# Optimization experiments

Hardware: AMD Instinct MI355X
Metric: run time of the kernel (lower is better)

## Reference

```python
import jax, jax.numpy as jnp
import numpy as np

K = 11          # kernel_size
SIGMA = 1.5
CH = 3          # image channels


def _gaussian_kernel(ch):
    coords = jnp.arange(K, dtype=jnp.float32) - (K - 1) / 2
    g = jnp.exp(-coords ** 2 / (2 * SIGMA ** 2))
    g = g / g.sum()
    k2d = jnp.outer(g, g)                       # [K, K]
    return jnp.tile(k2d[None, None], (ch, 1, 1, 1))  # [C, 1, K, K] depthwise


def setup_inputs() -> dict:
    key = jax.random.key(0)
    kx, ky = jax.random.split(key)
    x = jax.random.normal(kx, (32, CH, 512, 512), dtype=jnp.float32)
    y = jax.random.normal(ky, (32, CH, 512, 512), dtype=jnp.float32)
    kernel = _gaussian_kernel(CH)
    return {"x": x, "y": y, "kernel": kernel}


def _blur(v, kernel):
    # depthwise 2D Gaussian blur, SAME padding (K odd)
    c = v.shape[1]
    pad = K // 2
    return jax.lax.conv_general_dilated(
        v, kernel, window_strides=(1, 1), padding=[(pad, pad), (pad, pad)],
        dimension_numbers=("NCHW", "OIHW", "NCHW"), feature_group_count=c)


def reference(x, y, kernel):
    C1 = 0.01 ** 2
    C2 = 0.03 ** 2
    mu_x = _blur(x, kernel)
    mu_y = _blur(y, kernel)
    sigma_x = _blur(x * x, kernel) - mu_x ** 2
    sigma_y = _blur(y * y, kernel) - mu_y ** 2
    sigma_xy = _blur(x * y, kernel) - mu_x * mu_y
    ssim_num = (2 * mu_x * mu_y + C1) * (2 * sigma_xy + C2)
    ssim_den = (mu_x ** 2 + mu_y ** 2 + C1) * (sigma_x + sigma_y + C2)
    ssim = ssim_num / (ssim_den + 1e-8)
    return ((1.0 - ssim) / 2.0).mean()
```

## Files before the change

### kernel.cpp

```cpp
#include <hip/hip_runtime.h>
#include <hip/hip_bf16.h>

#define IMG    512
#define KSZ    11
#define HALO   5
#define STRIP  64
#define PANEL  16
#define FS     20
#define CS     100
#define WRSZ   1600

typedef short bf16x8 __attribute__((ext_vector_type(8)));
typedef float f32x4  __attribute__((ext_vector_type(4)));
union S8 { bf16x8 v; ushort u16[8]; uint u32[4]; };

__device__ __forceinline__ uint cvtpk(float lo, float hi) {
    uint r;
    asm("v_cvt_pk_bf16_f32 %0, %1, %2" : "=v"(r) : "v"(lo), "v"(hi));
    return r;
}
__device__ __forceinline__ float2 pk_mul(float2 a, float2 b) {
    float2 d;
    asm("v_pk_mul_f32 %0, %1, %2" : "=v"(d) : "v"(a), "v"(b));
    return d;
}
__device__ __forceinline__ ushort f2bf(float f) {
    union { __hip_bfloat16 h; ushort u; } c;
    c.h = __float2bfloat16(f);
    return c.u;
}


__global__ __launch_bounds__(256)
void dssim_mfma_kernel(const float* __restrict__ x,
                       const float* __restrict__ y,
                       const float* __restrict__ kern,
                       float* __restrict__ out)
{
    __shared__ float  sgf[16];
    __shared__ ushort gext[64];
    __shared__ __align__(16) uint Wring[4 * WRSZ];
    __shared__ float  wsum[4];

    const int tid = threadIdx.x;
    const int l   = tid & 63;
    const int wv  = tid >> 6;
    const int q   = l >> 4;
    const int cj  = l & 15;
    const int wb  = wv * WRSZ;

    if (tid < KSZ) {
        float s = 0.f;
        #pragma unroll
        for (int j = 0; j < KSZ; ++j) s += kern[tid * KSZ + j];
        sgf[tid] = s;
    }
    for (int i = l; i < 320; i += 64) {
        const int col = i / 20, r = i % 20, f = r >> 2, p = r & 3;
        Wring[wb + col * CS + f * FS + p] = 0u;
    }
    __syncthreads();
    if (tid < 64) {
        const int d = tid - 18;
        gext[tid] = (d >= 0 && d < KSZ) ? f2bf(sgf[d]) : (ushort)0;
    }
    __syncthreads();

    S8 tg;
    #pragma unroll
    for (int ii = 0; ii < 8; ++ii)
        tg.u16[ii] = gext[15 + q * 8 + ii - cj];

    const int plane  = blockIdx.z;
    const int half   = blockIdx.y;
    const int cstrip = blockIdx.x * STRIP;
    const int base   = plane * (IMG * IMG);

    const int  cb    = cstrip - 8 + 16 * wv + 8 * q;
    const bool colok = (cb >= 0) && (cb + 8 <= IMG);
    const float* xp  = x + base + cb;
    const float* yp  = y + base + cb;

    const int t0   = half ? 15 : 0;
    const int t1   = half ? 32 : 16;
    const int vmin = half ? 17 : 1;

    const f32x4 z0 = {0.f, 0.f, 0.f, 0.f};
    const float C1 = 1e-4f, C2 = 9e-4f;
    float local = 0.f;
    const int colbase = wb + cj * CS;

    int hg = (2 * t0 + 1 + (q >> 1)) % 5;
    int vg = (2 * t0 - 2 + q + 10) % 5;
    const int ho = 2 * (q & 1);

    f32x4 xa0, xb0, ya0, yb0, xa1, xb1, ya1, yb1;

    auto load8 = [&](int t, f32x4& xa, f32x4& xb, f32x4& ya, f32x4& yb) {
        const int r = t * PANEL + cj;
        if (r < IMG && colok) {
            const float* px = xp + r * IMG;
            const float* py = yp + r * IMG;
            xa = *(const f32x4*)px;  xb = *(const f32x4*)(px + 4);
            ya = *(const f32x4*)py;  yb = *(const f32x4*)(py + 4);
        } else {
            xa = z0; xb = z0; ya = z0; yb = z0;
        }
    };

    auto step = [&](int t, f32x4& xa, f32x4& xb, f32x4& ya, f32x4& yb) {
        float2 x01 = {xa[0], xa[1]}, x23 = {xa[2], xa[3]};
        float2 x45 = {xb[0], xb[1]}, x67 = {xb[2], xb[3]};
        float2 y01 = {ya[0], ya[1]}, y23 = {ya[2], ya[3]};
        float2 y45 = {yb[0], yb[1]}, y67 = {yb[2], yb[3]};
        S8 fx, fy, fxx, fyy, fxy;
        #pragma unroll
        for (int w = 0; w < 4; ++w) {
            const float2 xv = (w == 0) ? x01 : (w == 1) ? x23 : (w == 2) ? x45 : x67;
            const float2 yv = (w == 0) ? y01 : (w == 1) ? y23 : (w == 2) ? y45 : y67;
            const float2 xxv = pk_mul(xv, xv);
            const float2 yyv = pk_mul(yv, yv);
            const float2 xyv = pk_mul(xv, yv);
            fx .u32[w] = cvtpk(xv.x,  xv.y);
            fy .u32[w] = cvtpk(yv.x,  yv.y);
            fxx.u32[w] = cvtpk(xxv.x, xxv.y);
            fyy.u32[w] = cvtpk(yyv.x, yyv.y);
            fxy.u32[w] = cvtpk(xyv.x, xyv.y);
        }

        if (t + 2 <= t1) load8(t + 2, xa, xb, ya, yb);

        {
            const int hw = colbase + hg * 4 + ho;
            f32x4 d;
            uint2 w2;
            d = __builtin_amdgcn_mfma_f32_16x16x32_bf16(fx.v,  tg.v, z0, 0, 0, 0);
            w2.x = cvtpk(d[0], d[1]);  w2.y = cvtpk(d[2], d[3]);
            *(uint2*)&Wring[hw + 0 * FS] = w2;
            d = __builtin_amdgcn_mfma_f32_16x16x32_bf16(fy.v,  tg.v, z0, 0, 0, 0);
            w2.x = cvtpk(d[0], d[1]);  w2.y = cvtpk(d[2], d[3]);
            *(uint2*)&Wring[hw + 1 * FS] = w2;
            d = __builtin_amdgcn_mfma_f32_16x16x32_bf16(fxx.v, tg.v, z0, 0, 0, 0);
            w2.x = cvtpk(d[0], d[1]);  w2.y = cvtpk(d[2], d[3]);
            *(uint2*)&Wring[hw + 2 * FS] = w2;
            d = __builtin_amdgcn_mfma_f32_16x16x32_bf16(fyy.v, tg.v, z0, 0, 0, 0);
            w2.x = cvtpk(d[0], d[1]);  w2.y = cvtpk(d[2], d[3]);
            *(uint2*)&Wring[hw + 3 * FS] = w2;
            d = __builtin_amdgcn_mfma_f32_16x16x32_bf16(fxy.v, tg.v, z0, 0, 0, 0);
            w2.x = cvtpk(d[0], d[1]);  w2.y = cvtpk(d[2], d[3]);
            *(uint2*)&Wring[hw + 4 * FS] = w2;
        }

        if (t >= vmin) {
            const int vr = colbase + vg * 4;
            f32x4 vf[5];
            #pragma unroll
            for (int f = 0; f < 5; ++f) {
                const uint4 bb = *(const uint4*)&Wring[vr + f * FS];
                S8 b;
                b.u32[0] = bb.x; b.u32[1] = bb.y; b.u32[2] = bb.z; b.u32[3] = bb.w;
                vf[f] = __builtin_amdgcn_mfma_f32_16x16x32_bf16(tg.v, b.v, z0, 0, 0, 0);
            }
            #pragma unroll
            for (int r = 0; r < 4; ++r) {
                const float mx  = vf[0][r], my  = vf[1][r];
                const float exx = vf[2][r], eyy = vf[3][r], exy = vf[4][r];
                const float sxv = fmaf(-mx, mx, exx);
                const float syv = fmaf(-my, my, eyy);
                const float sxy = fmaf(-mx, my, exy);
                const float num = fmaf(2.f, mx * my, C1) * fmaf(2.f, sxy, C2);
                const float den = fmaf(mx, mx, fmaf(my, my, C1)) * (sxv + syv + C2);
                const float ssim = __fdividef(num, den + 1e-8f);
                local += (1.f - ssim) * 0.5f;
            }
        }

        hg += 2;  if (hg >= 5) hg -= 5;
        vg += 2;  if (vg >= 5) vg -= 5;
    };

    load8(t0,     xa0, xb0, ya0, yb0);
    load8(t0 + 1, xa1, xb1, ya1, yb1);

    for (int tt = t0; tt <= t1; tt += 2) {
        step(tt, xa0, xb0, ya0, yb0);
        if (tt + 1 <= t1) step(tt + 1, xa1, xb1, ya1, yb1);
    }

    #pragma unroll
    for (int o = 32; o > 0; o >>= 1) local += __shfl_down(local, o, 64);
    if (l == 0) wsum[wv] = local;
    __syncthreads();
    if (tid == 0) {
        const float s = wsum[0] + wsum[1] + wsum[2] + wsum[3];
        atomicAdd(out, s * (1.f / 25165824.f));
    }
}

extern "C" void kernel_launch(void* const* d_in, const int* in_sizes, int n_in,
                              void* d_out, int out_size, void* d_ws, size_t ws_size,
                              hipStream_t stream)
{
    const float* x    = (const float*)d_in[0];
    const float* y    = (const float*)d_in[1];
    const float* kern = (const float*)d_in[2];
    float* out = (float*)d_out;

    hipMemsetAsync(out, 0, sizeof(float), stream);

    dim3 grid(IMG / STRIP, 2, 32 * 3);
    dssim_mfma_kernel<<<grid, 256, 0, stream>>>(x, y, kern, out);
}
```

Measured before the change: 74.50 us.

## Blur sum/difference moments to cut MFMA planes from five to four

Rewrites SSIM in terms of s=x+y and d=x-y, so only four fields (s, d, s², d²) are blurred instead of five, which removes one horizontal and one vertical MFMA pass per panel and shrinks the LDS ring. The per-pixel (1-ssim)/2 is folded into a block-level constant term, and out-of-image row panels write zeros instead of loading. The risk is bf16 precision: s² and d² are larger than the original moments, and the variance is recovered by cancellation.

```diff
diff --git a/kernel.cpp b/kernel.cpp
--- a/kernel.cpp
+++ b/kernel.cpp
@@ -3,12 +3,11 @@
 
 #define IMG    512
 #define KSZ    11
-#define HALO   5
+#define PANEL  16
 #define STRIP  64
-#define PANEL  16
 #define FS     20
-#define CS     100
-#define WRSZ   1600
+#define CS     84
+#define WRSZ   (16 * CS)
 
 typedef short bf16x8 __attribute__((ext_vector_type(8)));
 typedef float f32x4  __attribute__((ext_vector_type(4)));
@@ -22,6 +21,16 @@
 __device__ __forceinline__ float2 pk_mul(float2 a, float2 b) {
     float2 d;
     asm("v_pk_mul_f32 %0, %1, %2" : "=v"(d) : "v"(a), "v"(b));
+    return d;
+}
+__device__ __forceinline__ float2 pk_add(float2 a, float2 b) {
+    float2 d;
+    asm("v_pk_add_f32 %0, %1, %2" : "=v"(d) : "v"(a), "v"(b));
+    return d;
+}
+__device__ __forceinline__ float2 pk_fma(float2 a, float2 b, float2 c) {
+    float2 d;
+    asm("v_pk_fma_f32 %0, %1, %2, %3" : "=v"(d) : "v"(a), "v"(b), "v"(c));
     return d;
 }
 __device__ __forceinline__ ushort f2bf(float f) {
@@ -55,8 +64,8 @@
         for (int j = 0; j < KSZ; ++j) s += kern[tid * KSZ + j];
         sgf[tid] = s;
     }
-    for (int i = l; i < 320; i += 64) {
-        const int col = i / 20, r = i % 20, f = r >> 2, p = r & 3;
+    for (int i = l; i < 256; i += 64) {
+        const int col = i >> 4, r = i & 15, f = r >> 2, p = r & 3;
         Wring[wb + col * CS + f * FS + p] = 0u;
     }
     __syncthreads();
@@ -78,15 +87,17 @@
 
     const int  cb    = cstrip - 8 + 16 * wv + 8 * q;
     const bool colok = (cb >= 0) && (cb + 8 <= IMG);
-    const float* xp  = x + base + cb;
-    const float* yp  = y + base + cb;
-
-    const int t0   = half ? 15 : 0;
-    const int t1   = half ? 32 : 16;
-    const int vmin = half ? 17 : 1;
+    const float* xl  = x + base + cb + cj * IMG;
+    const float* yl  = y + base + cb + cj * IMG;
+
+    const int t0    = half ? 15 : 0;
+    const int t1    = half ? 32 : 16;
+    const int hreal = half ? 31 : 16;
+    const int vmin  = half ? 17 : 1;
 
     const f32x4 z0 = {0.f, 0.f, 0.f, 0.f};
     const float C1 = 1e-4f, C2 = 9e-4f;
+    const float2 m1 = make_float2(-1.f, -1.f);
     float local = 0.f;
     const int colbase = wb + cj * CS;
 
@@ -97,10 +108,9 @@
     f32x4 xa0, xb0, ya0, yb0, xa1, xb1, ya1, yb1;
 
     auto load8 = [&](int t, f32x4& xa, f32x4& xb, f32x4& ya, f32x4& yb) {
-        const int r = t * PANEL + cj;
-        if (r < IMG && colok) {
-            const float* px = xp + r * IMG;
-            const float* py = yp + r * IMG;
+        const float* px = xl + t * (PANEL * IMG);
+        const float* py = yl + t * (PANEL * IMG);
+        if (colok) {
             xa = *(const f32x4*)px;  xb = *(const f32x4*)(px + 4);
             ya = *(const f32x4*)py;  yb = *(const f32x4*)(py + 4);
         } else {
@@ -109,53 +119,56 @@
     };
 
     auto step = [&](int t, f32x4& xa, f32x4& xb, f32x4& ya, f32x4& yb) {
-        float2 x01 = {xa[0], xa[1]}, x23 = {xa[2], xa[3]};
-        float2 x45 = {xb[0], xb[1]}, x67 = {xb[2], xb[3]};
-        float2 y01 = {ya[0], ya[1]}, y23 = {ya[2], ya[3]};
-        float2 y45 = {yb[0], yb[1]}, y67 = {yb[2], yb[3]};
-        S8 fx, fy, fxx, fyy, fxy;
-        #pragma unroll
-        for (int w = 0; w < 4; ++w) {
-            const float2 xv = (w == 0) ? x01 : (w == 1) ? x23 : (w == 2) ? x45 : x67;
-            const float2 yv = (w == 0) ? y01 : (w == 1) ? y23 : (w == 2) ? y45 : y67;
-            const float2 xxv = pk_mul(xv, xv);
-            const float2 yyv = pk_mul(yv, yv);
-            const float2 xyv = pk_mul(xv, yv);
-            fx .u32[w] = cvtpk(xv.x,  xv.y);
-            fy .u32[w] = cvtpk(yv.x,  yv.y);
-            fxx.u32[w] = cvtpk(xxv.x, xxv.y);
-            fyy.u32[w] = cvtpk(yyv.x, yyv.y);
-            fxy.u32[w] = cvtpk(xyv.x, xyv.y);
-        }
-
-        if (t + 2 <= t1) load8(t + 2, xa, xb, ya, yb);
-
-        {
-            const int hw = colbase + hg * 4 + ho;
+        const int hw = colbase + hg * 4 + ho;
+        if (t <= hreal) {
+            S8 fs, fd, fP, fM;
+            #pragma unroll
+            for (int w = 0; w < 4; ++w) {
+                const float2 xv = (w == 0) ? make_float2(xa[0], xa[1])
+                                : (w == 1) ? make_float2(xa[2], xa[3])
+                                : (w == 2) ? make_float2(xb[0], xb[1])
+                                :            make_float2(xb[2], xb[3]);
+                const float2 yv = (w == 0) ? make_float2(ya[0], ya[1])
+                                : (w == 1) ? make_float2(ya[2], ya[3])
+                                : (w == 2) ? make_float2(yb[0], yb[1])
+                                :            make_float2(yb[2], yb[3]);
+                const float2 sv = pk_add(xv, yv);
+                const float2 dv = pk_fma(yv, m1, xv);
+                const float2 Pv = pk_mul(sv, sv);
+                const float2 Mv = pk_mul(dv, dv);
+                fs.u32[w] = cvtpk(sv.x, sv.y);
+                fd.u32[w] = cvtpk(dv.x, dv.y);
+                fP.u32[w] = cvtpk(Pv.x, Pv.y);
+                fM.u32[w] = cvtpk(Mv.x, Mv.y);
+            }
+
+            if (t + 2 <= hreal) load8(t + 2, xa, xb, ya, yb);
+
             f32x4 d;
             uint2 w2;
-            d = __builtin_amdgcn_mfma_f32_16x16x32_bf16(fx.v,  tg.v, z0, 0, 0, 0);
+            d = __builtin_amdgcn_mfma_f32_16x16x32_bf16(fs.v, tg.v, z0, 0, 0, 0);
             w2.x = cvtpk(d[0], d[1]);  w2.y = cvtpk(d[2], d[3]);
             *(uint2*)&Wring[hw + 0 * FS] = w2;
-            d = __builtin_amdgcn_mfma_f32_16x16x32_bf16(fy.v,  tg.v, z0, 0, 0, 0);
+            d = __builtin_amdgcn_mfma_f32_16x16x32_bf16(fd.v, tg.v, z0, 0, 0, 0);
             w2.x = cvtpk(d[0], d[1]);  w2.y = cvtpk(d[2], d[3]);
             *(uint2*)&Wring[hw + 1 * FS] = w2;
-            d = __builtin_amdgcn_mfma_f32_16x16x32_bf16(fxx.v, tg.v, z0, 0, 0, 0);
+            d = __builtin_amdgcn_mfma_f32_16x16x32_bf16(fP.v, tg.v, z0, 0, 0, 0);
             w2.x = cvtpk(d[0], d[1]);  w2.y = cvtpk(d[2], d[3]);
             *(uint2*)&Wring[hw + 2 * FS] = w2;
-            d = __builtin_amdgcn_mfma_f32_16x16x32_bf16(fyy.v, tg.v, z0, 0, 0, 0);
+            d = __builtin_amdgcn_mfma_f32_16x16x32_bf16(fM.v, tg.v, z0, 0, 0, 0);
             w2.x = cvtpk(d[0], d[1]);  w2.y = cvtpk(d[2], d[3]);
             *(uint2*)&Wring[hw + 3 * FS] = w2;
-            d = __builtin_amdgcn_mfma_f32_16x16x32_bf16(fxy.v, tg.v, z0, 0, 0, 0);
-            w2.x = cvtpk(d[0], d[1]);  w2.y = cvtpk(d[2], d[3]);
-            *(uint2*)&Wring[hw + 4 * FS] = w2;
+        } else {
+            const uint2 zz = {0u, 0u};
+            #pragma unroll
+            for (int f = 0; f < 4; ++f) *(uint2*)&Wring[hw + f * FS] = zz;
         }
 
         if (t >= vmin) {
             const int vr = colbase + vg * 4;
-            f32x4 vf[5];
-            #pragma unroll
-            for (int f = 0; f < 5; ++f) {
+            f32x4 vf[4];
+            #pragma unroll
+            for (int f = 0; f < 4; ++f) {
                 const uint4 bb = *(const uint4*)&Wring[vr + f * FS];
                 S8 b;
                 b.u32[0] = bb.x; b.u32[1] = bb.y; b.u32[2] = bb.z; b.u32[3] = bb.w;
@@ -163,15 +176,15 @@
             }
             #pragma unroll
             for (int r = 0; r < 4; ++r) {
-                const float mx  = vf[0][r], my  = vf[1][r];
-                const float exx = vf[2][r], eyy = vf[3][r], exy = vf[4][r];
-                const float sxv = fmaf(-mx, mx, exx);
-                const float syv = fmaf(-my, my, eyy);
-                const float sxy = fmaf(-mx, my, exy);
-                const float num = fmaf(2.f, mx * my, C1) * fmaf(2.f, sxy, C2);
-                const float den = fmaf(mx, mx, fmaf(my, my, C1)) * (sxv + syv + C2);
-                const float ssim = __fdividef(num, den + 1e-8f);
-                local += (1.f - ssim) * 0.5f;
+                const float us = vf[0][r], ud = vf[1][r];
+                const float P  = vf[2][r], M  = vf[3][r];
+                const float u  = us * us, v = ud * ud;
+                const float a  = fmaf(0.5f, u - v, C1);
+                const float b  = fmaf(0.5f, u + v, C1);
+                const float ps = P - u,  md = M - v;
+                const float c  = fmaf(0.5f, ps - md, C2);
+                const float e  = fmaf(0.5f, ps + md, C2);
+                local += __fdividef(a * c, fmaf(b, e, 1e-8f));
             }
         }
 
@@ -192,8 +205,8 @@
     if (l == 0) wsum[wv] = local;
     __syncthreads();
     if (tid == 0) {
-        const float s = wsum[0] + wsum[1] + wsum[2] + wsum[3];
-        atomicAdd(out, s * (1.f / 25165824.f));
+        const float ssimsum = wsum[0] + wsum[1] + wsum[2] + wsum[3];
+        atomicAdd(out, (16384.f - ssimsum) * (0.5f / 25165824.f));
     }
 }
 
```

Result: slower. 76.04 us (+2.1%).
